# Optimization experiments

Hardware: AMD Instinct MI355X
Metric: run time of the kernel (lower is better)

The kernel has to match this reference:

```python
import jax, jax.numpy as jnp
import numpy as np

N = 50000      # nodes
F_IN = 512     # input features
HID = 128      # hidden
CLS = 64       # classes
E = 800000     # edges (avg degree 16)
EPS = 1e-5


def setup_inputs() -> dict:
    key = jax.random.key(0)
    k = jax.random.split(key, 6)
    x = jax.random.normal(k[0], (N, F_IN), jnp.float32)
    edge_index = jax.random.randint(k[1], (2, E), 0, N, dtype=jnp.int32)
    W1 = jax.random.normal(k[2], (F_IN, HID), jnp.float32) / np.float32(np.sqrt(F_IN))
    b1 = jnp.zeros((HID,), jnp.float32)
    W2 = jax.random.normal(k[3], (HID, CLS), jnp.float32) / np.float32(np.sqrt(HID))
    b2 = jnp.zeros((CLS,), jnp.float32)
    return {"x": x, "edge_index": edge_index, "W1": W1, "b1": b1, "W2": W2, "b2": b2}


def bin_active(x):
    # BinActive(scalar=True): per-node sign binarization scaled by mean |x| over features
    return jnp.sign(x) * jnp.mean(jnp.abs(x), axis=1, keepdims=True)


def bin_weight(w):
    # binarized weight with per-output-channel scaling (XNOR-style)
    return jnp.sign(w) * jnp.mean(jnp.abs(w), axis=0, keepdims=True)


def gcn_norm(edge_index, n):
    # add self-loops, symmetric D^-1/2 (A+I) D^-1/2 normalization (cached in original)
    loops = jnp.arange(n, dtype=edge_index.dtype)
    row = jnp.concatenate([edge_index[0], loops])  # source
    col = jnp.concatenate([edge_index[1], loops])  # target
    deg = jax.ops.segment_sum(jnp.ones(row.shape[0], jnp.float32), col, num_segments=n)
    dinv = jnp.where(deg > 0, jax.lax.rsqrt(jnp.maximum(deg, 1.0)), 0.0)
    return row, col, dinv[row] * dinv[col]


def bigcn_conv(x, W, b, row, col, norm, n):
    h = x @ bin_weight(W)                                   # [n, out]
    msg = norm[:, None] * h[row]                            # gather + scale, [E+n, out]
    return jax.ops.segment_sum(msg, col, num_segments=n) + b


def reference(x, edge_index, W1, b1, W2, b2):
    n = x.shape[0]
    # BatchNorm1d(affine=False), batch statistics (biased var)
    mu = jnp.mean(x, axis=0)
    var = jnp.var(x, axis=0)
    x = (x - mu) * jax.lax.rsqrt(var + EPS)
    row, col, norm = gcn_norm(edge_index, n)
    # layer loop: BinActive -> (dropout is identity in eval) -> BiGCNConv
    x = bigcn_conv(bin_active(x), W1, b1, row, col, norm, n)
    x = bigcn_conv(bin_active(x), W2, b2, row, col, norm, n)
    return jax.nn.log_softmax(x, axis=1)
```

## Files before the change

kernel.cpp:

```cpp
#include <hip/hip_runtime.h>

typedef unsigned long long u64;

#define F_IN 512
#define HID 128
#define CLS 64
#define EPS 1e-5f
#define NSB 512

__global__ __launch_bounds__(256) void col_stats_k(const float4* __restrict__ x4,
                                                   float* __restrict__ psum,
                                                   float* __restrict__ psq,
                                                   int n, int rpb) {
    __shared__ float red[256][9];
    int c4 = threadIdx.x & 127;
    int half = threadIdx.x >> 7;
    int r0 = blockIdx.x * rpb;
    int r1 = min(n, r0 + rpb);
    float s0=0.f,s1=0.f,s2=0.f,s3=0.f,q0=0.f,q1=0.f,q2=0.f,q3=0.f;
#pragma unroll 4
    for (int r = r0 + half; r < r1; r += 2) {
        float4 v = x4[(size_t)r * 128 + c4];
        s0 += v.x; q0 += v.x * v.x;
        s1 += v.y; q1 += v.y * v.y;
        s2 += v.z; q2 += v.z * v.z;
        s3 += v.w; q3 += v.w * v.w;
    }
    red[threadIdx.x][0]=s0; red[threadIdx.x][1]=s1; red[threadIdx.x][2]=s2; red[threadIdx.x][3]=s3;
    red[threadIdx.x][4]=q0; red[threadIdx.x][5]=q1; red[threadIdx.x][6]=q2; red[threadIdx.x][7]=q3;
    __syncthreads();
    if (half == 0) {
        int c = c4 * 4;
        float* os = &psum[(size_t)blockIdx.x * 512 + c];
        float* oq = &psq [(size_t)blockIdx.x * 512 + c];
        os[0] = s0 + red[c4+128][0]; os[1] = s1 + red[c4+128][1];
        os[2] = s2 + red[c4+128][2]; os[3] = s3 + red[c4+128][3];
        oq[0] = q0 + red[c4+128][4]; oq[1] = q1 + red[c4+128][5];
        oq[2] = q2 + red[c4+128][6]; oq[3] = q3 + red[c4+128][7];
    }
}

__global__ __launch_bounds__(256) void stats_reduce_k(const float* __restrict__ psum,
                                                      const float* __restrict__ psq,
                                                      float* __restrict__ mu,
                                                      float* __restrict__ rinv, int n) {
    __shared__ float reds[256], redq[256];
    int cc = threadIdx.x & 31;
    int bs = threadIdx.x >> 5;
    int c = blockIdx.x * 32 + cc;
    float s = 0.f, q = 0.f;
#pragma unroll 4
    for (int b = bs; b < NSB; b += 8) {
        s += psum[(size_t)b * 512 + c];
        q += psq [(size_t)b * 512 + c];
    }
    reds[threadIdx.x] = s; redq[threadIdx.x] = q;
    __syncthreads();
    if (bs == 0) {
#pragma unroll
        for (int t = 1; t < 8; ++t) { s += reds[cc + 32*t]; q += redq[cc + 32*t]; }
        float m = s / (float)n;
        float v = q / (float)n - m * m;
        mu[c] = m;
        rinv[c] = rsqrtf(v + EPS);
    }
}

__global__ __launch_bounds__(64) void pack_w1_k(const float* __restrict__ W,
                                                u64* __restrict__ sig,
                                                float* __restrict__ beta) {
    int j = blockIdx.x;
    int l = threadIdx.x;
    float asum = 0.f;
#pragma unroll
    for (int jw = 0; jw < 8; ++jw) {
        int f = (jw < 4) ? (4*l + jw) : (256 + 4*l + (jw - 4));
        float v = W[(size_t)f * HID + j];
        asum += fabsf(v);
        u64 b = __ballot(v > 0.0f);
        if (l == 0) sig[jw * HID + j] = b;
    }
    for (int m = 32; m >= 1; m >>= 1) asum += __shfl_xor(asum, m);
    if (l == 0) beta[j] = asum * (1.0f / 512.0f);
}

__global__ __launch_bounds__(64) void pack_w2_k(const float* __restrict__ W,
                                                ulonglong2* __restrict__ sigw2,
                                                float* __restrict__ beta2) {
    int j = blockIdx.x;
    int l = threadIdx.x;
    float v0 = W[(size_t)(2 * l) * CLS + j];
    float v1 = W[(size_t)(2 * l + 1) * CLS + j];
    float asum = fabsf(v0) + fabsf(v1);
    u64 s0 = __ballot(v0 > 0.0f);
    u64 s1 = __ballot(v1 > 0.0f);
    for (int m = 32; m >= 1; m >>= 1) asum += __shfl_xor(asum, m);
    if (l == 0) {
        ulonglong2 t; t.x = s0; t.y = s1;
        sigw2[j] = t;
        beta2[j] = asum * (1.0f / 128.0f);
    }
}

__global__ __launch_bounds__(256) void deg_k(const int* __restrict__ col,
                                             int* __restrict__ deg, int e) {
    int i = blockIdx.x * blockDim.x + threadIdx.x;
    if (i < e) atomicAdd(&deg[col[i]], 1);
}

__global__ __launch_bounds__(256) void scan_partial_k(const int* __restrict__ deg,
                                                      int* __restrict__ bsum, int n) {
    __shared__ int lds[256];
    int i = blockIdx.x * 256 + threadIdx.x;
    lds[threadIdx.x] = (i < n) ? deg[i] : 0;
    __syncthreads();
    for (int s = 128; s > 0; s >>= 1) {
        if (threadIdx.x < s) lds[threadIdx.x] += lds[threadIdx.x + s];
        __syncthreads();
    }
    if (threadIdx.x == 0) bsum[blockIdx.x] = lds[0];
}

__global__ __launch_bounds__(256) void scan_bsum_k(const int* __restrict__ bsum,
                                                   int* __restrict__ boff, int nb) {
    __shared__ int lds[256];
    int t = threadIdx.x;
    int v = (t < nb) ? bsum[t] : 0;
    lds[t] = v;
    __syncthreads();
    for (int s = 1; s < 256; s <<= 1) {
        int add = (t >= s) ? lds[t - s] : 0;
        __syncthreads();
        lds[t] += add;
        __syncthreads();
    }
    if (t < nb) boff[t] = lds[t] - v;
}

__global__ __launch_bounds__(256) void scan_final_k(const int* __restrict__ deg,
                                                    const int* __restrict__ boff,
                                                    int* __restrict__ offs,
                                                    int* __restrict__ cursor,
                                                    float* __restrict__ dinv, int n) {
    __shared__ int lds[256];
    int t = threadIdx.x;
    int i = blockIdx.x * 256 + t;
    int v = (i < n) ? deg[i] : 0;
    lds[t] = v;
    __syncthreads();
    for (int s = 1; s < 256; s <<= 1) {
        int add = (t >= s) ? lds[t - s] : 0;
        __syncthreads();
        lds[t] += add;
        __syncthreads();
    }
    int excl = lds[t] - v + boff[blockIdx.x];
    if (i < n) {
        offs[i] = excl; cursor[i] = excl;
        dinv[i] = rsqrtf((float)v + 1.0f);
    }
}

__global__ __launch_bounds__(256) void fill_k(const int* __restrict__ row,
                                              const int* __restrict__ col,
                                              const float* __restrict__ dinv,
                                              int* __restrict__ cursor,
                                              int2* __restrict__ csr, int e) {
    int i = blockIdx.x * blockDim.x + threadIdx.x;
    if (i < e) {
        int r = row[i], c = col[i];
        int p = atomicAdd(&cursor[c], 1);
        float w = dinv[r] * dinv[c];
        csr[p] = make_int2(r, __float_as_int(w));
    }
}

__global__ __launch_bounds__(256) void bin1_gemm1_k(const float4* __restrict__ x4,
                                                    const float4* __restrict__ mu4,
                                                    const float4* __restrict__ rinv4,
                                                    const u64* __restrict__ sigW,
                                                    float* __restrict__ a1,
                                                    short2* __restrict__ dots, int n) {
    int tid = threadIdx.x;
    int wave = tid >> 6, l = tid & 63;
    int i = blockIdx.x * 4 + wave;
    if (i >= n) return;
    const float4* xr = x4 + (size_t)i * 128;
    float4 va = xr[l], vb = xr[64 + l];
    float4 ma = mu4[l], mb = mu4[64 + l];
    float4 ra = rinv4[l], rb = rinv4[64 + l];
    float t0 = va.x - ma.x, t1 = va.y - ma.y, t2 = va.z - ma.z, t3 = va.w - ma.w;
    float t4 = vb.x - mb.x, t5 = vb.y - mb.y, t6 = vb.z - mb.z, t7 = vb.w - mb.w;
    float asum = fabsf(t0)*ra.x + fabsf(t1)*ra.y + fabsf(t2)*ra.z + fabsf(t3)*ra.w
               + fabsf(t4)*rb.x + fabsf(t5)*rb.y + fabsf(t6)*rb.z + fabsf(t7)*rb.w;
    u64 sx[8];
    sx[0] = __ballot(t0 > 0.f); sx[1] = __ballot(t1 > 0.f);
    sx[2] = __ballot(t2 > 0.f); sx[3] = __ballot(t3 > 0.f);
    sx[4] = __ballot(t4 > 0.f); sx[5] = __ballot(t5 > 0.f);
    sx[6] = __ballot(t6 > 0.f); sx[7] = __ballot(t7 > 0.f);
    for (int m = 32; m >= 1; m >>= 1) asum += __shfl_xor(asum, m);
    if (l == 0) a1[i] = asum * (1.0f / 512.0f);
    int c0 = 0, c1 = 0;
#pragma unroll
    for (int w = 0; w < 8; ++w) {
        c0 += __popcll(sx[w] ^ sigW[w * HID + 2*l]);
        c1 += __popcll(sx[w] ^ sigW[w * HID + 2*l + 1]);
    }
    dots[(size_t)i * 64 + l] = make_short2((short)(512 - 2*c0), (short)(512 - 2*c1));
}

__global__ __launch_bounds__(256) void agg1_fused_k(const short2* __restrict__ dots,
                                                    const float* __restrict__ a1,
                                                    const int2* __restrict__ csr,
                                                    const int* __restrict__ offs,
                                                    const int* __restrict__ deg,
                                                    const float* __restrict__ dinv,
                                                    const float2* __restrict__ beta1_2,
                                                    const float2* __restrict__ b1_2,
                                                    u64* __restrict__ sig2x,
                                                    float* __restrict__ a2v, int n) {
    int tid = threadIdx.x;
    int wave = tid >> 6, l = tid & 63;
    int i = blockIdx.x * 4 + wave;
    if (i >= n) return;
    float di = dinv[i];
    float ts = di * di * a1[i];
    short2 ds = dots[(size_t)i * 64 + l];
    float acc0 = ts * (float)ds.x;
    float acc1 = ts * (float)ds.y;
    int off = offs[i], d = deg[i];
    int k = 0;
    for (; k + 4 <= d; k += 4) {
        int2 e0 = csr[off+k], e1 = csr[off+k+1], e2 = csr[off+k+2], e3 = csr[off+k+3];
        float t0 = __int_as_float(e0.y) * a1[e0.x];
        float t1 = __int_as_float(e1.y) * a1[e1.x];
        float t2 = __int_as_float(e2.y) * a1[e2.x];
        float t3 = __int_as_float(e3.y) * a1[e3.x];
        short2 d0 = dots[(size_t)e0.x * 64 + l];
        short2 d1 = dots[(size_t)e1.x * 64 + l];
        short2 d2 = dots[(size_t)e2.x * 64 + l];
        short2 d3 = dots[(size_t)e3.x * 64 + l];
        acc0 += t0*(float)d0.x + t1*(float)d1.x + t2*(float)d2.x + t3*(float)d3.x;
        acc1 += t0*(float)d0.y + t1*(float)d1.y + t2*(float)d2.y + t3*(float)d3.y;
    }
    for (; k < d; ++k) {
        int2 ew = csr[off + k];
        float t = __int_as_float(ew.y) * a1[ew.x];
        short2 dv = dots[(size_t)ew.x * 64 + l];
        acc0 += t * (float)dv.x;
        acc1 += t * (float)dv.y;
    }
    float2 be = beta1_2[l], bb = b1_2[l];
    acc0 = be.x * acc0 + bb.x;
    acc1 = be.y * acc1 + bb.y;
    float asum = fabsf(acc0) + fabsf(acc1);
    for (int m = 32; m >= 1; m >>= 1) asum += __shfl_xor(asum, m);
    u64 s0 = __ballot(acc0 > 0.f);
    u64 s1 = __ballot(acc1 > 0.f);
    if (l == 0) {
        ulonglong2 pk; pk.x = s0; pk.y = s1;
        *(ulonglong2*)&sig2x[2 * (size_t)i] = pk;
        a2v[i] = asum * (1.0f / 128.0f);
    }
}

__global__ __launch_bounds__(256) void agg2_pop_k(const u64* __restrict__ sig2x,
                                                  const float* __restrict__ a2v,
                                                  const int2* __restrict__ csr,
                                                  const int* __restrict__ offs,
                                                  const int* __restrict__ deg,
                                                  const float* __restrict__ dinv,
                                                  const ulonglong2* __restrict__ sigw2,
                                                  const float* __restrict__ beta2,
                                                  const float* __restrict__ b2,
                                                  float* __restrict__ out, int n) {
    int tid = threadIdx.x;
    int wave = tid >> 6, l = tid & 63;
    int i = blockIdx.x * 4 + wave;
    if (i >= n) return;
    ulonglong2 wsig = sigw2[l];
    float bet = beta2[l], bias = b2[l];
    float di = dinv[i];
    float ts = di * di * a2v[i];
    ulonglong2 ss = *(const ulonglong2*)&sig2x[2 * (size_t)i];
    int dp = __popcll(ss.x ^ wsig.x) + __popcll(ss.y ^ wsig.y);
    float acc = ts * (float)(128 - 2 * dp);
    int off = offs[i], d = deg[i];
    int k = 0;
    for (; k + 4 <= d; k += 4) {
        int2 e0 = csr[off+k], e1 = csr[off+k+1], e2 = csr[off+k+2], e3 = csr[off+k+3];
        ulonglong2 g0 = *(const ulonglong2*)&sig2x[2 * (size_t)e0.x];
        ulonglong2 g1 = *(const ulonglong2*)&sig2x[2 * (size_t)e1.x];
        ulonglong2 g2 = *(const ulonglong2*)&sig2x[2 * (size_t)e2.x];
        ulonglong2 g3 = *(const ulonglong2*)&sig2x[2 * (size_t)e3.x];
        float t0 = __int_as_float(e0.y) * a2v[e0.x];
        float t1 = __int_as_float(e1.y) * a2v[e1.x];
        float t2 = __int_as_float(e2.y) * a2v[e2.x];
        float t3 = __int_as_float(e3.y) * a2v[e3.x];
        int p0 = __popcll(g0.x ^ wsig.x) + __popcll(g0.y ^ wsig.y);
        int p1 = __popcll(g1.x ^ wsig.x) + __popcll(g1.y ^ wsig.y);
        int p2 = __popcll(g2.x ^ wsig.x) + __popcll(g2.y ^ wsig.y);
        int p3 = __popcll(g3.x ^ wsig.x) + __popcll(g3.y ^ wsig.y);
        acc += t0 * (float)(128 - 2*p0) + t1 * (float)(128 - 2*p1)
             + t2 * (float)(128 - 2*p2) + t3 * (float)(128 - 2*p3);
    }
    for (; k < d; ++k) {
        int2 ew = csr[off + k];
        ulonglong2 gs = *(const ulonglong2*)&sig2x[2 * (size_t)ew.x];
        float t = __int_as_float(ew.y) * a2v[ew.x];
        int p = __popcll(gs.x ^ wsig.x) + __popcll(gs.y ^ wsig.y);
        acc += t * (float)(128 - 2*p);
    }
    float o = bet * acc + bias;
    float m = o;
    for (int k2 = 32; k2 >= 1; k2 >>= 1) m = fmaxf(m, __shfl_xor(m, k2));
    float ev = __expf(o - m);
    float s = ev;
    for (int k2 = 32; k2 >= 1; k2 >>= 1) s += __shfl_xor(s, k2);
    out[(size_t)i * CLS + l] = o - m - __logf(s);
}

extern "C" void kernel_launch(void* const* d_in, const int* in_sizes, int n_in,
                              void* d_out, int out_size, void* d_ws, size_t ws_size,
                              hipStream_t stream) {
    const float* x  = (const float*)d_in[0];
    const int*   ei = (const int*)d_in[1];
    const float* W1 = (const float*)d_in[2];
    const float* b1 = (const float*)d_in[3];
    const float* W2 = (const float*)d_in[4];
    const float* b2 = (const float*)d_in[5];
    float* out = (float*)d_out;

    const int n = in_sizes[0] / F_IN;
    const int e = in_sizes[1] / 2;
    const int* row = ei;
    const int* col = ei + e;

    char* w = (char*)d_ws;
    size_t off = 0;
    auto alloc = [&](size_t bytes) {
        void* p = w + off;
        off += (bytes + 255) & ~(size_t)255;
        return p;
    };
    int*   deg    = (int*)alloc((size_t)n * 4);
    size_t zero_bytes = off;
    float* psum   = (float*)alloc((size_t)NSB * 512 * 4);
    float* psq    = (float*)alloc((size_t)NSB * 512 * 4);
    float* mu     = (float*)alloc(F_IN * 4);
    float* rinv   = (float*)alloc(F_IN * 4);
    float* dinv   = (float*)alloc((size_t)n * 4);
    float* beta1  = (float*)alloc(HID * 4);
    u64*   sig1   = (u64*)alloc(HID * 8 * 8);
    ulonglong2* sigw2 = (ulonglong2*)alloc(CLS * 16);
    float* beta2  = (float*)alloc(CLS * 4);
    int*   offs   = (int*)alloc((size_t)n * 4);
    int*   cursor = (int*)alloc((size_t)n * 4);
    int*   bsum   = (int*)alloc(256 * 4);
    int*   boff   = (int*)alloc(256 * 4);
    int2*  csr    = (int2*)alloc((size_t)e * 8);
    short2* dots  = (short2*)alloc((size_t)n * 64 * 4);
    float* a1     = (float*)alloc((size_t)n * 4);
    u64*   sig2x  = (u64*)alloc((size_t)n * 2 * 8);
    float* a2v    = (float*)alloc((size_t)n * 4);
    (void)ws_size;

    hipMemsetAsync(d_ws, 0, zero_bytes, stream);

    int rpb = (n + NSB - 1) / NSB;
    col_stats_k<<<NSB, 256, 0, stream>>>((const float4*)x, psum, psq, n, rpb);
    stats_reduce_k<<<16, 256, 0, stream>>>(psum, psq, mu, rinv, n);
    pack_w1_k<<<HID, 64, 0, stream>>>(W1, sig1, beta1);
    pack_w2_k<<<CLS, 64, 0, stream>>>(W2, sigw2, beta2);
    deg_k<<<(e + 255) / 256, 256, 0, stream>>>(col, deg, e);

    int nb = (n + 255) / 256;
    scan_partial_k<<<nb, 256, 0, stream>>>(deg, bsum, n);
    scan_bsum_k<<<1, 256, 0, stream>>>(bsum, boff, nb);
    scan_final_k<<<nb, 256, 0, stream>>>(deg, boff, offs, cursor, dinv, n);

    bin1_gemm1_k<<<(n + 3) / 4, 256, 0, stream>>>((const float4*)x, (const float4*)mu,
                                                  (const float4*)rinv, sig1, a1, dots, n);
    fill_k<<<(e + 255) / 256, 256, 0, stream>>>(row, col, dinv, cursor, csr, e);
    agg1_fused_k<<<(n + 3) / 4, 256, 0, stream>>>(dots, a1, csr, offs, deg, dinv,
                                                  (const float2*)beta1, (const float2*)b1,
                                                  sig2x, a2v, n);
    agg2_pop_k<<<(n + 3) / 4, 256, 0, stream>>>(sig2x, a2v, csr, offs, deg, dinv,
                                                sigw2, beta2, b2, out, n);
}
```

Before: 384.9 us.

## Merge independent prep kernels into block-dispatched launches and unroll gathers by eight

Independent stages (column stats, degree counting, W1/W2 packing) are merged into one launch that dispatches on block index. Stats reduction is merged with the partial scan, and binarize-GEMM1 with CSR fill, cutting the launch count from 12 to 7. The memset now starts at deg instead of the workspace base. Both aggregation loops are unrolled from 4 to 8 edges with loads batched ahead of use, to put more gathers in flight at the cost of extra registers.

After: 360.8 us. -6.3%, faster.

```diff
diff --git a/kernel.cpp b/kernel.cpp
--- a/kernel.cpp
+++ b/kernel.cpp
@@ -8,117 +8,122 @@
 #define EPS 1e-5f
 #define NSB 512
 
-__global__ __launch_bounds__(256) void col_stats_k(const float4* __restrict__ x4,
-                                                   float* __restrict__ psum,
-                                                   float* __restrict__ psq,
-                                                   int n, int rpb) {
+__global__ __launch_bounds__(256) void prep_k(const float4* __restrict__ x4,
+                                              float* __restrict__ psum,
+                                              float* __restrict__ psq,
+                                              int n, int rpb,
+                                              const int* __restrict__ col,
+                                              int* __restrict__ deg, int e, int nbdeg,
+                                              const float* __restrict__ W1,
+                                              u64* __restrict__ sig1,
+                                              float* __restrict__ beta1,
+                                              const float* __restrict__ W2,
+                                              ulonglong2* __restrict__ sigw2,
+                                              float* __restrict__ beta2) {
     __shared__ float red[256][9];
-    int c4 = threadIdx.x & 127;
-    int half = threadIdx.x >> 7;
-    int r0 = blockIdx.x * rpb;
-    int r1 = min(n, r0 + rpb);
-    float s0=0.f,s1=0.f,s2=0.f,s3=0.f,q0=0.f,q1=0.f,q2=0.f,q3=0.f;
+    int b = blockIdx.x;
+    int tid = threadIdx.x;
+    if (b < NSB) {
+        int c4 = tid & 127;
+        int half = tid >> 7;
+        int r0 = b * rpb;
+        int r1 = min(n, r0 + rpb);
+        float s0=0.f,s1=0.f,s2=0.f,s3=0.f,q0=0.f,q1=0.f,q2=0.f,q3=0.f;
 #pragma unroll 4
-    for (int r = r0 + half; r < r1; r += 2) {
-        float4 v = x4[(size_t)r * 128 + c4];
-        s0 += v.x; q0 += v.x * v.x;
-        s1 += v.y; q1 += v.y * v.y;
-        s2 += v.z; q2 += v.z * v.z;
-        s3 += v.w; q3 += v.w * v.w;
-    }
-    red[threadIdx.x][0]=s0; red[threadIdx.x][1]=s1; red[threadIdx.x][2]=s2; red[threadIdx.x][3]=s3;
-    red[threadIdx.x][4]=q0; red[threadIdx.x][5]=q1; red[threadIdx.x][6]=q2; red[threadIdx.x][7]=q3;
-    __syncthreads();
-    if (half == 0) {
-        int c = c4 * 4;
-        float* os = &psum[(size_t)blockIdx.x * 512 + c];
-        float* oq = &psq [(size_t)blockIdx.x * 512 + c];
-        os[0] = s0 + red[c4+128][0]; os[1] = s1 + red[c4+128][1];
-        os[2] = s2 + red[c4+128][2]; os[3] = s3 + red[c4+128][3];
-        oq[0] = q0 + red[c4+128][4]; oq[1] = q1 + red[c4+128][5];
-        oq[2] = q2 + red[c4+128][6]; oq[3] = q3 + red[c4+128][7];
-    }
-}
-
-__global__ __launch_bounds__(256) void stats_reduce_k(const float* __restrict__ psum,
-                                                      const float* __restrict__ psq,
-                                                      float* __restrict__ mu,
-                                                      float* __restrict__ rinv, int n) {
+        for (int r = r0 + half; r < r1; r += 2) {
+            float4 v = x4[(size_t)r * 128 + c4];
+            s0 += v.x; q0 += v.x * v.x;
+            s1 += v.y; q1 += v.y * v.y;
+            s2 += v.z; q2 += v.z * v.z;
+            s3 += v.w; q3 += v.w * v.w;
+        }
+        red[tid][0]=s0; red[tid][1]=s1; red[tid][2]=s2; red[tid][3]=s3;
+        red[tid][4]=q0; red[tid][5]=q1; red[tid][6]=q2; red[tid][7]=q3;
+        __syncthreads();
+        if (half == 0) {
+            int c = c4 * 4;
+            float* os = &psum[(size_t)b * 512 + c];
+            float* oq = &psq [(size_t)b * 512 + c];
+            os[0] = s0 + red[c4+128][0]; os[1] = s1 + red[c4+128][1];
+            os[2] = s2 + red[c4+128][2]; os[3] = s3 + red[c4+128][3];
+            oq[0] = q0 + red[c4+128][4]; oq[1] = q1 + red[c4+128][5];
+            oq[2] = q2 + red[c4+128][6]; oq[3] = q3 + red[c4+128][7];
+        }
+    } else if (b < NSB + nbdeg) {
+        int i = (b - NSB) * 256 + tid;
+        if (i < e) atomicAdd(&deg[col[i]], 1);
+    } else if (b < NSB + nbdeg + 32) {
+        int wave = tid >> 6, l = tid & 63;
+        int j = (b - NSB - nbdeg) * 4 + wave;
+        float asum = 0.f;
+#pragma unroll
+        for (int jw = 0; jw < 8; ++jw) {
+            int f = (jw < 4) ? (4*l + jw) : (256 + 4*l + (jw - 4));
+            float v = W1[(size_t)f * HID + j];
+            asum += fabsf(v);
+            u64 bb = __ballot(v > 0.0f);
+            if (l == 0) sig1[jw * HID + j] = bb;
+        }
+        for (int m = 32; m >= 1; m >>= 1) asum += __shfl_xor(asum, m);
+        if (l == 0) beta1[j] = asum * (1.0f / 512.0f);
+    } else {
+        int wave = tid >> 6, l = tid & 63;
+        int j = (b - NSB - nbdeg - 32) * 4 + wave;
+        float v0 = W2[(size_t)(2 * l) * CLS + j];
+        float v1 = W2[(size_t)(2 * l + 1) * CLS + j];
+        float asum = fabsf(v0) + fabsf(v1);
+        u64 s0 = __ballot(v0 > 0.0f);
+        u64 s1 = __ballot(v1 > 0.0f);
+        for (int m = 32; m >= 1; m >>= 1) asum += __shfl_xor(asum, m);
+        if (l == 0) {
+            ulonglong2 t; t.x = s0; t.y = s1;
+            sigw2[j] = t;
+            beta2[j] = asum * (1.0f / 128.0f);
+        }
+    }
+}
+
+__global__ __launch_bounds__(256) void mid_k(const float* __restrict__ psum,
+                                             const float* __restrict__ psq,
+                                             float* __restrict__ mu,
+                                             float* __restrict__ rinv, int n,
+                                             const int* __restrict__ deg,
+                                             int* __restrict__ bsum) {
     __shared__ float reds[256], redq[256];
-    int cc = threadIdx.x & 31;
-    int bs = threadIdx.x >> 5;
-    int c = blockIdx.x * 32 + cc;
-    float s = 0.f, q = 0.f;
+    __shared__ int lds[256];
+    int b = blockIdx.x;
+    int t = threadIdx.x;
+    if (b < 16) {
+        int cc = t & 31;
+        int bs = t >> 5;
+        int c = b * 32 + cc;
+        float s = 0.f, q = 0.f;
 #pragma unroll 4
-    for (int b = bs; b < NSB; b += 8) {
-        s += psum[(size_t)b * 512 + c];
-        q += psq [(size_t)b * 512 + c];
-    }
-    reds[threadIdx.x] = s; redq[threadIdx.x] = q;
-    __syncthreads();
-    if (bs == 0) {
-#pragma unroll
-        for (int t = 1; t < 8; ++t) { s += reds[cc + 32*t]; q += redq[cc + 32*t]; }
-        float m = s / (float)n;
-        float v = q / (float)n - m * m;
-        mu[c] = m;
-        rinv[c] = rsqrtf(v + EPS);
-    }
-}
-
-__global__ __launch_bounds__(64) void pack_w1_k(const float* __restrict__ W,
-                                                u64* __restrict__ sig,
-                                                float* __restrict__ beta) {
-    int j = blockIdx.x;
-    int l = threadIdx.x;
-    float asum = 0.f;
-#pragma unroll
-    for (int jw = 0; jw < 8; ++jw) {
-        int f = (jw < 4) ? (4*l + jw) : (256 + 4*l + (jw - 4));
-        float v = W[(size_t)f * HID + j];
-        asum += fabsf(v);
-        u64 b = __ballot(v > 0.0f);
-        if (l == 0) sig[jw * HID + j] = b;
-    }
-    for (int m = 32; m >= 1; m >>= 1) asum += __shfl_xor(asum, m);
-    if (l == 0) beta[j] = asum * (1.0f / 512.0f);
-}
-
-__global__ __launch_bounds__(64) void pack_w2_k(const float* __restrict__ W,
-                                                ulonglong2* __restrict__ sigw2,
-                                                float* __restrict__ beta2) {
-    int j = blockIdx.x;
-    int l = threadIdx.x;
-    float v0 = W[(size_t)(2 * l) * CLS + j];
-    float v1 = W[(size_t)(2 * l + 1) * CLS + j];
-    float asum = fabsf(v0) + fabsf(v1);
-    u64 s0 = __ballot(v0 > 0.0f);
-    u64 s1 = __ballot(v1 > 0.0f);
-    for (int m = 32; m >= 1; m >>= 1) asum += __shfl_xor(asum, m);
-    if (l == 0) {
-        ulonglong2 t; t.x = s0; t.y = s1;
-        sigw2[j] = t;
-        beta2[j] = asum * (1.0f / 128.0f);
-    }
-}
-
-__global__ __launch_bounds__(256) void deg_k(const int* __restrict__ col,
-                                             int* __restrict__ deg, int e) {
-    int i = blockIdx.x * blockDim.x + threadIdx.x;
-    if (i < e) atomicAdd(&deg[col[i]], 1);
-}
-
-__global__ __launch_bounds__(256) void scan_partial_k(const int* __restrict__ deg,
-                                                      int* __restrict__ bsum, int n) {
-    __shared__ int lds[256];
-    int i = blockIdx.x * 256 + threadIdx.x;
-    lds[threadIdx.x] = (i < n) ? deg[i] : 0;
-    __syncthreads();
-    for (int s = 128; s > 0; s >>= 1) {
-        if (threadIdx.x < s) lds[threadIdx.x] += lds[threadIdx.x + s];
-        __syncthreads();
-    }
-    if (threadIdx.x == 0) bsum[blockIdx.x] = lds[0];
+        for (int p = bs; p < NSB; p += 8) {
+            s += psum[(size_t)p * 512 + c];
+            q += psq [(size_t)p * 512 + c];
+        }
+        reds[t] = s; redq[t] = q;
+        __syncthreads();
+        if (bs == 0) {
+#pragma unroll
+            for (int u = 1; u < 8; ++u) { s += reds[cc + 32*u]; q += redq[cc + 32*u]; }
+            float m = s / (float)n;
+            float v = q / (float)n - m * m;
+            mu[c] = m;
+            rinv[c] = rsqrtf(v + EPS);
+        }
+    } else {
+        int blk = b - 16;
+        int i = blk * 256 + t;
+        lds[t] = (i < n) ? deg[i] : 0;
+        __syncthreads();
+        for (int s = 128; s > 0; s >>= 1) {
+            if (t < s) lds[t] += lds[t + s];
+            __syncthreads();
+        }
+        if (t == 0) bsum[blk] = lds[0];
+    }
 }
 
 __global__ __launch_bounds__(256) void scan_bsum_k(const int* __restrict__ bsum,
@@ -161,52 +166,54 @@
     }
 }
 
-__global__ __launch_bounds__(256) void fill_k(const int* __restrict__ row,
-                                              const int* __restrict__ col,
-                                              const float* __restrict__ dinv,
-                                              int* __restrict__ cursor,
-                                              int2* __restrict__ csr, int e) {
-    int i = blockIdx.x * blockDim.x + threadIdx.x;
-    if (i < e) {
-        int r = row[i], c = col[i];
-        int p = atomicAdd(&cursor[c], 1);
-        float w = dinv[r] * dinv[c];
-        csr[p] = make_int2(r, __float_as_int(w));
-    }
-}
-
-__global__ __launch_bounds__(256) void bin1_gemm1_k(const float4* __restrict__ x4,
-                                                    const float4* __restrict__ mu4,
-                                                    const float4* __restrict__ rinv4,
-                                                    const u64* __restrict__ sigW,
-                                                    float* __restrict__ a1,
-                                                    short2* __restrict__ dots, int n) {
+__global__ __launch_bounds__(256) void main1_k(const float4* __restrict__ x4,
+                                               const float4* __restrict__ mu4,
+                                               const float4* __restrict__ rinv4,
+                                               const u64* __restrict__ sigW,
+                                               float* __restrict__ a1,
+                                               short2* __restrict__ dots, int n, int nbin,
+                                               const int* __restrict__ row,
+                                               const int* __restrict__ col,
+                                               const float* __restrict__ dinv,
+                                               int* __restrict__ cursor,
+                                               int2* __restrict__ csr, int e) {
+    int b = blockIdx.x;
     int tid = threadIdx.x;
-    int wave = tid >> 6, l = tid & 63;
-    int i = blockIdx.x * 4 + wave;
-    if (i >= n) return;
-    const float4* xr = x4 + (size_t)i * 128;
-    float4 va = xr[l], vb = xr[64 + l];
-    float4 ma = mu4[l], mb = mu4[64 + l];
-    float4 ra = rinv4[l], rb = rinv4[64 + l];
-    float t0 = va.x - ma.x, t1 = va.y - ma.y, t2 = va.z - ma.z, t3 = va.w - ma.w;
-    float t4 = vb.x - mb.x, t5 = vb.y - mb.y, t6 = vb.z - mb.z, t7 = vb.w - mb.w;
-    float asum = fabsf(t0)*ra.x + fabsf(t1)*ra.y + fabsf(t2)*ra.z + fabsf(t3)*ra.w
-               + fabsf(t4)*rb.x + fabsf(t5)*rb.y + fabsf(t6)*rb.z + fabsf(t7)*rb.w;
-    u64 sx[8];
-    sx[0] = __ballot(t0 > 0.f); sx[1] = __ballot(t1 > 0.f);
-    sx[2] = __ballot(t2 > 0.f); sx[3] = __ballot(t3 > 0.f);
-    sx[4] = __ballot(t4 > 0.f); sx[5] = __ballot(t5 > 0.f);
-    sx[6] = __ballot(t6 > 0.f); sx[7] = __ballot(t7 > 0.f);
-    for (int m = 32; m >= 1; m >>= 1) asum += __shfl_xor(asum, m);
-    if (l == 0) a1[i] = asum * (1.0f / 512.0f);
-    int c0 = 0, c1 = 0;
-#pragma unroll
-    for (int w = 0; w < 8; ++w) {
-        c0 += __popcll(sx[w] ^ sigW[w * HID + 2*l]);
-        c1 += __popcll(sx[w] ^ sigW[w * HID + 2*l + 1]);
-    }
-    dots[(size_t)i * 64 + l] = make_short2((short)(512 - 2*c0), (short)(512 - 2*c1));
+    if (b < nbin) {
+        int wave = tid >> 6, l = tid & 63;
+        int i = b * 4 + wave;
+        if (i >= n) return;
+        const float4* xr = x4 + (size_t)i * 128;
+        float4 va = xr[l], vb = xr[64 + l];
+        float4 ma = mu4[l], mb = mu4[64 + l];
+        float4 ra = rinv4[l], rb = rinv4[64 + l];
+        float t0 = va.x - ma.x, t1 = va.y - ma.y, t2 = va.z - ma.z, t3 = va.w - ma.w;
+        float t4 = vb.x - mb.x, t5 = vb.y - mb.y, t6 = vb.z - mb.z, t7 = vb.w - mb.w;
+        float asum = fabsf(t0)*ra.x + fabsf(t1)*ra.y + fabsf(t2)*ra.z + fabsf(t3)*ra.w
+                   + fabsf(t4)*rb.x + fabsf(t5)*rb.y + fabsf(t6)*rb.z + fabsf(t7)*rb.w;
+        u64 sx[8];
+        sx[0] = __ballot(t0 > 0.f); sx[1] = __ballot(t1 > 0.f);
+        sx[2] = __ballot(t2 > 0.f); sx[3] = __ballot(t3 > 0.f);
+        sx[4] = __ballot(t4 > 0.f); sx[5] = __ballot(t5 > 0.f);
+        sx[6] = __ballot(t6 > 0.f); sx[7] = __ballot(t7 > 0.f);
+        for (int m = 32; m >= 1; m >>= 1) asum += __shfl_xor(asum, m);
+        if (l == 0) a1[i] = asum * (1.0f / 512.0f);
+        int c0 = 0, c1 = 0;
+#pragma unroll
+        for (int w = 0; w < 8; ++w) {
+            c0 += __popcll(sx[w] ^ sigW[w * HID + 2*l]);
+            c1 += __popcll(sx[w] ^ sigW[w * HID + 2*l + 1]);
+        }
+        dots[(size_t)i * 64 + l] = make_short2((short)(512 - 2*c0), (short)(512 - 2*c1));
+    } else {
+        int i = (b - nbin) * 256 + tid;
+        if (i < e) {
+            int r = row[i], c = col[i];
+            int p = atomicAdd(&cursor[c], 1);
+            float w = dinv[r] * dinv[c];
+            csr[p] = make_int2(r, __float_as_int(w));
+        }
+    }
 }
 
 __global__ __launch_bounds__(256) void agg1_fused_k(const short2* __restrict__ dots,
@@ -230,18 +237,19 @@
     float acc1 = ts * (float)ds.y;
     int off = offs[i], d = deg[i];
     int k = 0;
-    for (; k + 4 <= d; k += 4) {
-        int2 e0 = csr[off+k], e1 = csr[off+k+1], e2 = csr[off+k+2], e3 = csr[off+k+3];
-        float t0 = __int_as_float(e0.y) * a1[e0.x];
-        float t1 = __int_as_float(e1.y) * a1[e1.x];
-        float t2 = __int_as_float(e2.y) * a1[e2.x];
-        float t3 = __int_as_float(e3.y) * a1[e3.x];
-        short2 d0 = dots[(size_t)e0.x * 64 + l];
-        short2 d1 = dots[(size_t)e1.x * 64 + l];
-        short2 d2 = dots[(size_t)e2.x * 64 + l];
-        short2 d3 = dots[(size_t)e3.x * 64 + l];
-        acc0 += t0*(float)d0.x + t1*(float)d1.x + t2*(float)d2.x + t3*(float)d3.x;
-        acc1 += t0*(float)d0.y + t1*(float)d1.y + t2*(float)d2.y + t3*(float)d3.y;
+    for (; k + 8 <= d; k += 8) {
+        int2 ee[8]; float tt[8]; short2 dd[8];
+#pragma unroll
+        for (int u = 0; u < 8; ++u) ee[u] = csr[off + k + u];
+#pragma unroll
+        for (int u = 0; u < 8; ++u) tt[u] = __int_as_float(ee[u].y) * a1[ee[u].x];
+#pragma unroll
+        for (int u = 0; u < 8; ++u) dd[u] = dots[(size_t)ee[u].x * 64 + l];
+#pragma unroll
+        for (int u = 0; u < 8; ++u) {
+            acc0 += tt[u] * (float)dd[u].x;
+            acc1 += tt[u] * (float)dd[u].y;
+        }
     }
     for (; k < d; ++k) {
         int2 ew = csr[off + k];
@@ -287,29 +295,26 @@
     float acc = ts * (float)(128 - 2 * dp);
     int off = offs[i], d = deg[i];
     int k = 0;
-    for (; k + 4 <= d; k += 4) {
-        int2 e0 = csr[off+k], e1 = csr[off+k+1], e2 = csr[off+k+2], e3 = csr[off+k+3];
-        ulonglong2 g0 = *(const ulonglong2*)&sig2x[2 * (size_t)e0.x];
-        ulonglong2 g1 = *(const ulonglong2*)&sig2x[2 * (size_t)e1.x];
-        ulonglong2 g2 = *(const ulonglong2*)&sig2x[2 * (size_t)e2.x];
-        ulonglong2 g3 = *(const ulonglong2*)&sig2x[2 * (size_t)e3.x];
-        float t0 = __int_as_float(e0.y) * a2v[e0.x];
-        float t1 = __int_as_float(e1.y) * a2v[e1.x];
-        float t2 = __int_as_float(e2.y) * a2v[e2.x];
-        float t3 = __int_as_float(e3.y) * a2v[e3.x];
-        int p0 = __popcll(g0.x ^ wsig.x) + __popcll(g0.y ^ wsig.y);
-        int p1 = __popcll(g1.x ^ wsig.x) + __popcll(g1.y ^ wsig.y);
-        int p2 = __popcll(g2.x ^ wsig.x) + __popcll(g2.y ^ wsig.y);
-        int p3 = __popcll(g3.x ^ wsig.x) + __popcll(g3.y ^ wsig.y);
-        acc += t0 * (float)(128 - 2*p0) + t1 * (float)(128 - 2*p1)
-             + t2 * (float)(128 - 2*p2) + t3 * (float)(128 - 2*p3);
+    for (; k + 8 <= d; k += 8) {
+        int2 ee[8]; float tt[8]; ulonglong2 gg[8];
+#pragma unroll
+        for (int u = 0; u < 8; ++u) ee[u] = csr[off + k + u];
+#pragma unroll
+        for (int u = 0; u < 8; ++u) tt[u] = __int_as_float(ee[u].y) * a2v[ee[u].x];
+#pragma unroll
+        for (int u = 0; u < 8; ++u) gg[u] = *(const ulonglong2*)&sig2x[2 * (size_t)ee[u].x];
+#pragma unroll
+        for (int u = 0; u < 8; ++u) {
+            int p = __popcll(gg[u].x ^ wsig.x) + __popcll(gg[u].y ^ wsig.y);
+            acc += tt[u] * (float)(128 - 2 * p);
+        }
     }
     for (; k < d; ++k) {
         int2 ew = csr[off + k];
         ulonglong2 gs = *(const ulonglong2*)&sig2x[2 * (size_t)ew.x];
         float t = __int_as_float(ew.y) * a2v[ew.x];
         int p = __popcll(gs.x ^ wsig.x) + __popcll(gs.y ^ wsig.y);
-        acc += t * (float)(128 - 2*p);
+        acc += t * (float)(128 - 2 * p);
     }
     float o = bet * acc + bias;
     float m = o;
@@ -365,26 +370,29 @@
     float* a2v    = (float*)alloc((size_t)n * 4);
     (void)ws_size;
 
-    hipMemsetAsync(d_ws, 0, zero_bytes, stream);
+    hipMemsetAsync(deg, 0, zero_bytes, stream);
 
     int rpb = (n + NSB - 1) / NSB;
-    col_stats_k<<<NSB, 256, 0, stream>>>((const float4*)x, psum, psq, n, rpb);
-    stats_reduce_k<<<16, 256, 0, stream>>>(psum, psq, mu, rinv, n);
-    pack_w1_k<<<HID, 64, 0, stream>>>(W1, sig1, beta1);
-    pack_w2_k<<<CLS, 64, 0, stream>>>(W2, sigw2, beta2);
-    deg_k<<<(e + 255) / 256, 256, 0, stream>>>(col, deg, e);
-
+    int nbdeg = (e + 255) / 256;
     int nb = (n + 255) / 256;
-    scan_partial_k<<<nb, 256, 0, stream>>>(deg, bsum, n);
+    int nbin = (n + 3) / 4;
+
+    prep_k<<<NSB + nbdeg + 32 + 16, 256, 0, stream>>>(
+        (const float4*)x, psum, psq, n, rpb,
+        col, deg, e, nbdeg,
+        W1, sig1, beta1, W2, sigw2, beta2);
+
+    mid_k<<<16 + nb, 256, 0, stream>>>(psum, psq, mu, rinv, n, deg, bsum);
     scan_bsum_k<<<1, 256, 0, stream>>>(bsum, boff, nb);
     scan_final_k<<<nb, 256, 0, stream>>>(deg, boff, offs, cursor, dinv, n);
 
-    bin1_gemm1_k<<<(n + 3) / 4, 256, 0, stream>>>((const float4*)x, (const float4*)mu,
-                                                  (const float4*)rinv, sig1, a1, dots, n);
-    fill_k<<<(e + 255) / 256, 256, 0, stream>>>(row, col, dinv, cursor, csr, e);
-    agg1_fused_k<<<(n + 3) / 4, 256, 0, stream>>>(dots, a1, csr, offs, deg, dinv,
-                                                  (const float2*)beta1, (const float2*)b1,
-                                                  sig2x, a2v, n);
-    agg2_pop_k<<<(n + 3) / 4, 256, 0, stream>>>(sig2x, a2v, csr, offs, deg, dinv,
-                                                sigw2, beta2, b2, out, n);
-}
+    main1_k<<<nbin + nbdeg, 256, 0, stream>>>(
+        (const float4*)x, (const float4*)mu, (const float4*)rinv, sig1, a1, dots, n, nbin,
+        row, col, dinv, cursor, csr, e);
+
+    agg1_fused_k<<<nbin, 256, 0, stream>>>(dots, a1, csr, offs, deg, dinv,
+                                           (const float2*)beta1, (const float2*)b1,
+                                           sig2x, a2v, n);
+    agg2_pop_k<<<nbin, 256, 0, stream>>>(sig2x, a2v, csr, offs, deg, dinv,
+                                         sigw2, beta2, b2, out, n);
+}
```
